# Optimization experiments

Measured on AMD Instinct MI355X. Metric: run time of the kernel, lower is better.

The kernel has to match this reference:

```python
import jax, jax.numpy as jnp
import numpy as np

SCALE = 0.08838834764831845  # 1/sqrt(128)


def setup_inputs() -> dict:
    key = jax.random.key(0)
    k1, k2, k3, k4 = jax.random.split(key, 4)
    B, Sq, H, D = 1, 2048, 32, 128
    Skv, K = 4096, 256
    return {
        "q": jax.random.normal(k1, (B, Sq, H, D), jnp.float32),
        "kv": jax.random.normal(k2, (B, Skv, 2, D), jnp.float32),  # stacked K,V (MQA)
        "attn_sink": jax.random.normal(k3, (H,), jnp.float32),
        "topk_idxs": jax.random.randint(k4, (B, Sq, K), 0, Skv),
    }


def reference(q, kv, attn_sink, topk_idxs):
    # q:        [B, Sq, H, D]
    # kv:       [B, Skv, 2, D]  (index 0 = keys, 1 = values; shared across heads)
    # topk_idxs:[B, Sq, K]      per-query selected KV positions
    # attn_sink:[H]             per-head sink logit added to the softmax denominator
    B = q.shape[0]
    # Gather selected KV per query: [B, Sq, K, 2, D]
    gathered = kv[jnp.arange(B)[:, None, None], topk_idxs]
    k = gathered[..., 0, :]  # [B, Sq, K, D]
    v = gathered[..., 1, :]  # [B, Sq, K, D]

    scores = jnp.einsum("bqhd,bqkd->bqhk", q, k) * SCALE  # [B, Sq, H, K]
    sink = attn_sink[None, None, :, None]                  # [1, 1, H, 1]

    # Numerically stable softmax over K selected tokens + sink logit.
    m = jnp.maximum(jnp.max(scores, axis=-1, keepdims=True), sink)
    e = jnp.exp(scores - m)
    denom = jnp.sum(e, axis=-1, keepdims=True) + jnp.exp(sink - m)
    probs = e / denom                                      # sink absorbs leftover mass

    out = jnp.einsum("bqhk,bqkd->bqhd", probs, v)          # [B, Sq, H, D]
    return out
```

## Files before the change

### kernel.cpp

```cpp
#include <hip/hip_runtime.h>
#include <hip/hip_bf16.h>

#define SQ 2048
#define NH 32
#define DH 128
#define NK 256
#define SCALE 0.08838834764831845f
#define LOG2E 1.4426950408889634f

typedef __attribute__((ext_vector_type(8))) __bf16 bf16x8;
typedef __attribute__((ext_vector_type(4))) float floatx4;

#define QS_STRIDE 136
#define KS_STRIDE 136
#define VB_STRIDE 72
#define PB_STRIDE 264

#define OFF_DB0  16896
#define DBSZ     18432
#define OFF_DB1  (OFF_DB0 + DBSZ)
#define OFF_RED  (OFF_DB1 + 17408)
#define OFF_RED2 (OFF_RED + 512)
#define SMEM_SZ  53760

#define SCHED_PIN() __builtin_amdgcn_sched_barrier(0)

__device__ __forceinline__ unsigned pk_bf16(float a, float b) {
  union { __hip_bfloat162 h2; unsigned u; } c;
  c.h2 = __float22bfloat162_rn(make_float2(a, b));
  return c.u;
}

__device__ __forceinline__ float fast_exp2(float x) {
#if __has_builtin(__builtin_amdgcn_exp2f)
  return __builtin_amdgcn_exp2f(x);
#else
  return exp2f(x);
#endif
}

template <int CTRL>
__device__ __forceinline__ float dpp_rot(float x) {
  int i = __builtin_bit_cast(int, x);
  i = __builtin_amdgcn_mov_dpp(i, CTRL, 0xF, 0xF, true);
  return __builtin_bit_cast(float, i);
}
#define RED16_MAX(v) { v = fmaxf(v, dpp_rot<0x121>(v)); v = fmaxf(v, dpp_rot<0x122>(v)); \
                       v = fmaxf(v, dpp_rot<0x124>(v)); v = fmaxf(v, dpp_rot<0x128>(v)); }
#define RED16_SUM(v) { v += dpp_rot<0x121>(v); v += dpp_rot<0x122>(v); \
                       v += dpp_rot<0x124>(v); v += dpp_rot<0x128>(v); }

__global__ __launch_bounds__(256) void kv_to_bf16(const float* __restrict__ kv,
                                                  unsigned short* __restrict__ kvb) {
  int i = blockIdx.x * 256 + threadIdx.x;
  float4 f = ((const float4*)kv)[i];
  uint2 o = { pk_bf16(f.x, f.y), pk_bf16(f.z, f.w) };
  ((uint2*)kvb)[i] = o;
}

struct KR { uint4 v[4]; };
struct VR { uint4 a, b, c, d; };

__device__ __forceinline__ KR k_load(const unsigned short* __restrict__ kvb,
                                     const int* __restrict__ tkg, int c, int tid) {
  int r = tid >> 2, seg = tid & 3;
  int idx = tkg[c * 64 + r];
  const uint4* p = (const uint4*)(kvb + (size_t)idx * 256 + seg * 32);
  KR k;
#pragma unroll
  for (int i = 0; i < 4; i++) k.v[i] = p[i];
  return k;
}

__device__ __forceinline__ void k_write(unsigned short* kbuf, const KR& k, int tid) {
  int r = tid >> 2, seg = tid & 3;
  uint4* d = (uint4*)&kbuf[r * KS_STRIDE + seg * 32];
#pragma unroll
  for (int i = 0; i < 4; i++) d[i] = k.v[i];
}

__device__ __forceinline__ VR v_load(const unsigned short* __restrict__ kvb,
                                     const int* __restrict__ tkg, int c, int tid) {
  int rg = tid & 15, dg = tid >> 4;
  int r0 = rg * 4, d0 = dg * 8;
  int4 i4 = *(const int4*)&tkg[c * 64 + r0];
  VR v;
  v.a = *(const uint4*)(kvb + (size_t)i4.x * 256 + 128 + d0);
  v.b = *(const uint4*)(kvb + (size_t)i4.y * 256 + 128 + d0);
  v.c = *(const uint4*)(kvb + (size_t)i4.z * 256 + 128 + d0);
  v.d = *(const uint4*)(kvb + (size_t)i4.w * 256 + 128 + d0);
  return v;
}

__device__ __forceinline__ void v_write(unsigned short* vbuf, const VR& v, int tid) {
  int rg = tid & 15, dg = tid >> 4;
  int r0 = rg * 4, d0 = dg * 8;
  const unsigned* pa = (const unsigned*)&v.a;
  const unsigned* pb = (const unsigned*)&v.b;
  const unsigned* pc = (const unsigned*)&v.c;
  const unsigned* pd = (const unsigned*)&v.d;
#pragma unroll
  for (int w = 0; w < 4; w++) {
    unsigned lo01 = __builtin_amdgcn_perm(pb[w], pa[w], 0x05040100u);
    unsigned lo23 = __builtin_amdgcn_perm(pd[w], pc[w], 0x05040100u);
    unsigned hi01 = __builtin_amdgcn_perm(pb[w], pa[w], 0x07060302u);
    unsigned hi23 = __builtin_amdgcn_perm(pd[w], pc[w], 0x07060302u);
    uint2 lo = { lo01, lo23 }, hi = { hi01, hi23 };
    *(uint2*)&vbuf[(d0 + 2 * w) * VB_STRIDE + r0] = lo;
    *(uint2*)&vbuf[(d0 + 2 * w + 1) * VB_STRIDE + r0] = hi;
  }
}

__device__ __forceinline__ void gemm1(const unsigned short* kbuf,
                                      const bf16x8 af[2][4], int nrow, int quad,
                                      floatx4& a0, floatx4& a1) {
  a0 = (floatx4){0.f, 0.f, 0.f, 0.f};
  a1 = (floatx4){0.f, 0.f, 0.f, 0.f};
  __builtin_amdgcn_s_setprio(1);
#pragma unroll
  for (int ks = 0; ks < 4; ks++) {
    bf16x8 b = *(const bf16x8*)&kbuf[nrow * KS_STRIDE + ks * 32 + quad * 8];
    a0 = __builtin_amdgcn_mfma_f32_16x16x32_bf16(af[0][ks], b, a0, 0, 0, 0);
    a1 = __builtin_amdgcn_mfma_f32_16x16x32_bf16(af[1][ks], b, a1, 0, 0, 0);
  }
  __builtin_amdgcn_s_setprio(0);
}

__device__ __forceinline__ void pv_chunk(const unsigned short* pbuf,
                                         const unsigned short* vbuf, int c,
                                         int wave, int quad, int l16,
                                         floatx4 oacc[2][2]) {
  __builtin_amdgcn_s_setprio(1);
#pragma unroll
  for (int ks = 0; ks < 2; ks++) {
    int kof = c * 64 + ks * 32 + quad * 8;
    bf16x8 a0 = *(const bf16x8*)&pbuf[l16 * PB_STRIDE + kof];
    bf16x8 a1 = *(const bf16x8*)&pbuf[(16 + l16) * PB_STRIDE + kof];
    int kl = ks * 32 + quad * 8;
    bf16x8 b0 = *(const bf16x8*)&vbuf[(wave * 32 + l16) * VB_STRIDE + kl];
    bf16x8 b1 = *(const bf16x8*)&vbuf[(wave * 32 + 16 + l16) * VB_STRIDE + kl];
    oacc[0][0] = __builtin_amdgcn_mfma_f32_16x16x32_bf16(a0, b0, oacc[0][0], 0, 0, 0);
    oacc[0][1] = __builtin_amdgcn_mfma_f32_16x16x32_bf16(a0, b1, oacc[0][1], 0, 0, 0);
    oacc[1][0] = __builtin_amdgcn_mfma_f32_16x16x32_bf16(a1, b0, oacc[1][0], 0, 0, 0);
    oacc[1][1] = __builtin_amdgcn_mfma_f32_16x16x32_bf16(a1, b1, oacc[1][1], 0, 0, 0);
  }
  __builtin_amdgcn_s_setprio(0);
}

__global__ __launch_bounds__(256, 3) void sparse_attn_kernel(
    const float* __restrict__ q, const unsigned short* __restrict__ kvb,
    const float* __restrict__ sink, const int* __restrict__ topk,
    float* __restrict__ out) {
  __shared__ __align__(16) char smem[SMEM_SZ];
  unsigned short* pbuf = (unsigned short*)smem;
  unsigned short* qs   = (unsigned short*)smem;
  unsigned short* db0  = (unsigned short*)(smem + OFF_DB0);
  unsigned short* db1  = (unsigned short*)(smem + OFF_DB1);
  float* red  = (float*)(smem + OFF_RED);
  float* red2 = (float*)(smem + OFF_RED2);

  const int tid = threadIdx.x;
  const int s = blockIdx.x;
  const int wave = tid >> 6;
  const int lane = tid & 63;
  const int quad = lane >> 4;
  const int l16 = lane & 15;
  const int* tkg = topk + (size_t)s * NK;
  unsigned short* dbuf[2] = { db0, db1 };

  {
    int r = tid >> 2, seg = tid & 3;
    int idx = tkg[r];
    const uint4* p = (const uint4*)(kvb + (size_t)idx * 256 + seg * 32);
    uint4* d = (uint4*)&db0[r * KS_STRIDE + seg * 32];
#pragma unroll
    for (int i = 0; i < 4; i++) d[i] = p[i];
  }
  KR k1 = k_load(kvb, tkg, 1, tid);
  SCHED_PIN();

  float snk[2][4];
#pragma unroll
  for (int mt = 0; mt < 2; mt++)
#pragma unroll
    for (int r = 0; r < 4; r++)
      snk[mt][r] = sink[mt * 16 + quad * 4 + r] * LOG2E;

  {
    const float QSC = SCALE * LOG2E;
    const float* qp = q + (size_t)s * (NH * DH);
    int h = tid >> 3, d0 = (tid & 7) * 16;
    const float4* src = (const float4*)(qp + h * DH + d0);
    float4 f0 = src[0], f1 = src[1], f2 = src[2], f3 = src[3];
    uint4 o0 = { pk_bf16(f0.x * QSC, f0.y * QSC), pk_bf16(f0.z * QSC, f0.w * QSC),
                 pk_bf16(f1.x * QSC, f1.y * QSC), pk_bf16(f1.z * QSC, f1.w * QSC) };
    uint4 o1 = { pk_bf16(f2.x * QSC, f2.y * QSC), pk_bf16(f2.z * QSC, f2.w * QSC),
                 pk_bf16(f3.x * QSC, f3.y * QSC), pk_bf16(f3.z * QSC, f3.w * QSC) };
    *(uint4*)&qs[h * QS_STRIDE + d0] = o0;
    *(uint4*)&qs[h * QS_STRIDE + d0 + 8] = o1;
  }
  __syncthreads();

  bf16x8 afrag[2][4];
#pragma unroll
  for (int mt = 0; mt < 2; mt++)
#pragma unroll
    for (int ks = 0; ks < 4; ks++)
      afrag[mt][ks] =
          *(const bf16x8*)&qs[(mt * 16 + l16) * QS_STRIDE + ks * 32 + quad * 8];

  const int nrow = wave * 16 + l16;

  floatx4 sc[4][2];
  KR k2 = k_load(kvb, tkg, 2, tid);
  SCHED_PIN();
  gemm1(dbuf[0], afrag, nrow, quad, sc[0][0], sc[0][1]);
  k_write(dbuf[1], k1, tid);
  __syncthreads();

  KR k3 = k_load(kvb, tkg, 3, tid);
  SCHED_PIN();
  gemm1(dbuf[1], afrag, nrow, quad, sc[1][0], sc[1][1]);
  k_write(dbuf[0], k2, tid);
  __syncthreads();

  VR v0 = v_load(kvb, tkg, 0, tid);
  SCHED_PIN();
  gemm1(dbuf[0], afrag, nrow, quad, sc[2][0], sc[2][1]);
  k_write(dbuf[1], k3, tid);
  __syncthreads();

  VR v1 = v_load(kvb, tkg, 1, tid);
  SCHED_PIN();
  gemm1(dbuf[1], afrag, nrow, quad, sc[3][0], sc[3][1]);
  v_write(dbuf[0], v0, tid);

  float mh[2][4];
#pragma unroll
  for (int mt = 0; mt < 2; mt++)
#pragma unroll
    for (int r = 0; r < 4; r++) {
      float v = fmaxf(fmaxf(sc[0][mt][r], sc[1][mt][r]),
                      fmaxf(sc[2][mt][r], sc[3][mt][r]));
      RED16_MAX(v);
      mh[mt][r] = v;
    }
  float ps[2][4];
#pragma unroll
  for (int mt = 0; mt < 2; mt++)
#pragma unroll
    for (int r = 0; r < 4; r++) {
      float acc = 0.f;
#pragma unroll
      for (int c = 0; c < 4; c++) {
        float e = fast_exp2(sc[c][mt][r] - mh[mt][r]);
        sc[c][mt][r] = e;
        acc += e;
      }
      RED16_SUM(acc);
      ps[mt][r] = acc;
    }
  if (l16 == 0) {
#pragma unroll
    for (int mt = 0; mt < 2; mt++)
#pragma unroll
      for (int r = 0; r < 4; r++) {
        red[wave * 32 + mt * 16 + quad * 4 + r]  = mh[mt][r];
        red2[wave * 32 + mt * 16 + quad * 4 + r] = ps[mt][r];
      }
  }
  __syncthreads();
  VR v2 = v_load(kvb, tkg, 2, tid);
  SCHED_PIN();
  float inv[2][4], sf[2][4];
#pragma unroll
  for (int mt = 0; mt < 2; mt++)
#pragma unroll
    for (int r = 0; r < 4; r++) {
      int h = mt * 16 + quad * 4 + r;
      float M = snk[mt][r];
#pragma unroll
      for (int w = 0; w < 4; w++) M = fmaxf(M, red[w * 32 + h]);
      float dd = fast_exp2(snk[mt][r] - M);
#pragma unroll
      for (int w = 0; w < 4; w++)
        dd += red2[w * 32 + h] * fast_exp2(red[w * 32 + h] - M);
      inv[mt][r] = 1.0f / dd;
      sf[mt][r] = fast_exp2(mh[mt][r] - M);
    }
#pragma unroll
  for (int c = 0; c < 4; c++)
#pragma unroll
    for (int mt = 0; mt < 2; mt++) {
      int col = c * 64 + wave * 16 + l16;
      unsigned short* pb = &pbuf[(mt * 16 + quad * 4) * PB_STRIDE + col];
      unsigned p01 = pk_bf16(sc[c][mt][0] * sf[mt][0], sc[c][mt][1] * sf[mt][1]);
      unsigned p23 = pk_bf16(sc[c][mt][2] * sf[mt][2], sc[c][mt][3] * sf[mt][3]);
      pb[0] = (unsigned short)p01;
      pb[PB_STRIDE] = (unsigned short)(p01 >> 16);
      pb[2 * PB_STRIDE] = (unsigned short)p23;
      pb[3 * PB_STRIDE] = (unsigned short)(p23 >> 16);
    }
  __syncthreads();

  floatx4 oacc[2][2];
#pragma unroll
  for (int mt = 0; mt < 2; mt++)
#pragma unroll
    for (int nt = 0; nt < 2; nt++)
      oacc[mt][nt] = (floatx4){0.f, 0.f, 0.f, 0.f};

  VR v3 = v_load(kvb, tkg, 3, tid);
  SCHED_PIN();
  pv_chunk(pbuf, dbuf[0], 0, wave, quad, l16, oacc);
  v_write(dbuf[1], v1, tid);
  __syncthreads();

  pv_chunk(pbuf, dbuf[1], 1, wave, quad, l16, oacc);
  v_write(dbuf[0], v2, tid);
  __syncthreads();

  pv_chunk(pbuf, dbuf[0], 2, wave, quad, l16, oacc);
  v_write(dbuf[1], v3, tid);
  __syncthreads();

  pv_chunk(pbuf, dbuf[1], 3, wave, quad, l16, oacc);

  {
    float* op = out + (size_t)s * (NH * DH);
#pragma unroll
    for (int mt = 0; mt < 2; mt++)
#pragma unroll
      for (int nt = 0; nt < 2; nt++)
#pragma unroll
        for (int r4 = 0; r4 < 4; r4++) {
          int h = mt * 16 + quad * 4 + r4;
          int d = wave * 32 + nt * 16 + l16;
          op[h * DH + d] = oacc[mt][nt][r4] * inv[mt][r4];
        }
  }
}

extern "C" void kernel_launch(void* const* d_in, const int* in_sizes, int n_in,
                              void* d_out, int out_size, void* d_ws, size_t ws_size,
                              hipStream_t stream) {
  (void)in_sizes; (void)n_in; (void)out_size; (void)ws_size;
  const float* q    = (const float*)d_in[0];
  const float* kv   = (const float*)d_in[1];
  const float* sink = (const float*)d_in[2];
  const int*   topk = (const int*)d_in[3];
  float* out = (float*)d_out;
  unsigned short* kvb = (unsigned short*)d_ws;

  kv_to_bf16<<<dim3(1024), dim3(256), 0, stream>>>(kv, kvb);
  sparse_attn_kernel<<<dim3(SQ), dim3(256), 0, stream>>>(q, kvb, sink, topk, out);
}
```

Baseline: 117.6 us.

## Load K fragments directly into registers and swizzle the probability buffer

K rows are now loaded straight from global memory into MFMA B-operand registers, with each lane fetching its own row, instead of being staged through double-buffered LDS. This removes the K LDS writes and reads plus three block barriers in the QK phase. The P buffer moves from a padded stride to an XOR-swizzled 512-byte row layout to avoid LDS bank conflicts. In exchange, register pressure rises because four K fragment sets are held at once, and the global loads are less coalesced since each lane reads 16B pieces of a gathered row.

```diff
diff --git a/kernel.cpp b/kernel.cpp
--- a/kernel.cpp
+++ b/kernel.cpp
@@ -12,18 +12,17 @@
 typedef __attribute__((ext_vector_type(4))) float floatx4;
 
 #define QS_STRIDE 136
-#define KS_STRIDE 136
 #define VB_STRIDE 72
-#define PB_STRIDE 264
-
-#define OFF_DB0  16896
-#define DBSZ     18432
-#define OFF_DB1  (OFF_DB0 + DBSZ)
-#define OFF_RED  (OFF_DB1 + 17408)
+
+#define OFF_DB0  16384
+#define OFF_DB1  (OFF_DB0 + 18432)
+#define OFF_RED  (OFF_DB1 + 18432)
 #define OFF_RED2 (OFF_RED + 512)
-#define SMEM_SZ  53760
+#define SMEM_SZ  54272
 
 #define SCHED_PIN() __builtin_amdgcn_sched_barrier(0)
+
+__device__ __forceinline__ int swz(int row) { return ((row ^ (row >> 3)) & 7) << 4; }
 
 __device__ __forceinline__ unsigned pk_bf16(float a, float b) {
   union { __hip_bfloat162 h2; unsigned u; } c;
@@ -58,26 +57,31 @@
   ((uint2*)kvb)[i] = o;
 }
 
-struct KR { uint4 v[4]; };
+struct KB { bf16x8 b[4]; };
+
+__device__ __forceinline__ KB kb_load(const unsigned short* __restrict__ kvb,
+                                      int idx, int quad) {
+  const unsigned short* kp = kvb + (size_t)idx * 256 + quad * 8;
+  KB k;
+#pragma unroll
+  for (int ks = 0; ks < 4; ks++) k.b[ks] = *(const bf16x8*)(kp + ks * 32);
+  return k;
+}
+
+__device__ __forceinline__ void gemm_reg(const KB& kb, const bf16x8 af[2][4],
+                                         floatx4& a0, floatx4& a1) {
+  a0 = (floatx4){0.f, 0.f, 0.f, 0.f};
+  a1 = (floatx4){0.f, 0.f, 0.f, 0.f};
+  __builtin_amdgcn_s_setprio(1);
+#pragma unroll
+  for (int ks = 0; ks < 4; ks++) {
+    a0 = __builtin_amdgcn_mfma_f32_16x16x32_bf16(af[0][ks], kb.b[ks], a0, 0, 0, 0);
+    a1 = __builtin_amdgcn_mfma_f32_16x16x32_bf16(af[1][ks], kb.b[ks], a1, 0, 0, 0);
+  }
+  __builtin_amdgcn_s_setprio(0);
+}
+
 struct VR { uint4 a, b, c, d; };
-
-__device__ __forceinline__ KR k_load(const unsigned short* __restrict__ kvb,
-                                     const int* __restrict__ tkg, int c, int tid) {
-  int r = tid >> 2, seg = tid & 3;
-  int idx = tkg[c * 64 + r];
-  const uint4* p = (const uint4*)(kvb + (size_t)idx * 256 + seg * 32);
-  KR k;
-#pragma unroll
-  for (int i = 0; i < 4; i++) k.v[i] = p[i];
-  return k;
-}
-
-__device__ __forceinline__ void k_write(unsigned short* kbuf, const KR& k, int tid) {
-  int r = tid >> 2, seg = tid & 3;
-  uint4* d = (uint4*)&kbuf[r * KS_STRIDE + seg * 32];
-#pragma unroll
-  for (int i = 0; i < 4; i++) d[i] = k.v[i];
-}
 
 __device__ __forceinline__ VR v_load(const unsigned short* __restrict__ kvb,
                                      const int* __restrict__ tkg, int c, int tid) {
@@ -111,31 +115,16 @@
   }
 }
 
-__device__ __forceinline__ void gemm1(const unsigned short* kbuf,
-                                      const bf16x8 af[2][4], int nrow, int quad,
-                                      floatx4& a0, floatx4& a1) {
-  a0 = (floatx4){0.f, 0.f, 0.f, 0.f};
-  a1 = (floatx4){0.f, 0.f, 0.f, 0.f};
-  __builtin_amdgcn_s_setprio(1);
-#pragma unroll
-  for (int ks = 0; ks < 4; ks++) {
-    bf16x8 b = *(const bf16x8*)&kbuf[nrow * KS_STRIDE + ks * 32 + quad * 8];
-    a0 = __builtin_amdgcn_mfma_f32_16x16x32_bf16(af[0][ks], b, a0, 0, 0, 0);
-    a1 = __builtin_amdgcn_mfma_f32_16x16x32_bf16(af[1][ks], b, a1, 0, 0, 0);
-  }
-  __builtin_amdgcn_s_setprio(0);
-}
-
-__device__ __forceinline__ void pv_chunk(const unsigned short* pbuf,
+__device__ __forceinline__ void pv_chunk(const char* pbuf,
                                          const unsigned short* vbuf, int c,
                                          int wave, int quad, int l16,
                                          floatx4 oacc[2][2]) {
   __builtin_amdgcn_s_setprio(1);
 #pragma unroll
   for (int ks = 0; ks < 2; ks++) {
-    int kof = c * 64 + ks * 32 + quad * 8;
-    bf16x8 a0 = *(const bf16x8*)&pbuf[l16 * PB_STRIDE + kof];
-    bf16x8 a1 = *(const bf16x8*)&pbuf[(16 + l16) * PB_STRIDE + kof];
+    int kof = (c * 64 + ks * 32 + quad * 8) * 2;
+    bf16x8 a0 = *(const bf16x8*)(pbuf + ((l16 * 512 + kof) ^ swz(l16)));
+    bf16x8 a1 = *(const bf16x8*)(pbuf + (((16 + l16) * 512 + kof) ^ swz(16 + l16)));
     int kl = ks * 32 + quad * 8;
     bf16x8 b0 = *(const bf16x8*)&vbuf[(wave * 32 + l16) * VB_STRIDE + kl];
     bf16x8 b1 = *(const bf16x8*)&vbuf[(wave * 32 + 16 + l16) * VB_STRIDE + kl];
@@ -152,10 +141,10 @@
     const float* __restrict__ sink, const int* __restrict__ topk,
     float* __restrict__ out) {
   __shared__ __align__(16) char smem[SMEM_SZ];
-  unsigned short* pbuf = (unsigned short*)smem;
-  unsigned short* qs   = (unsigned short*)smem;
-  unsigned short* db0  = (unsigned short*)(smem + OFF_DB0);
-  unsigned short* db1  = (unsigned short*)(smem + OFF_DB1);
+  char* pbuf = smem;
+  unsigned short* qs  = (unsigned short*)smem;
+  unsigned short* db0 = (unsigned short*)(smem + OFF_DB0);
+  unsigned short* db1 = (unsigned short*)(smem + OFF_DB1);
   float* red  = (float*)(smem + OFF_RED);
   float* red2 = (float*)(smem + OFF_RED2);
 
@@ -166,17 +155,13 @@
   const int quad = lane >> 4;
   const int l16 = lane & 15;
   const int* tkg = topk + (size_t)s * NK;
-  unsigned short* dbuf[2] = { db0, db1 };
-
-  {
-    int r = tid >> 2, seg = tid & 3;
-    int idx = tkg[r];
-    const uint4* p = (const uint4*)(kvb + (size_t)idx * 256 + seg * 32);
-    uint4* d = (uint4*)&db0[r * KS_STRIDE + seg * 32];
-#pragma unroll
-    for (int i = 0; i < 4; i++) d[i] = p[i];
-  }
-  KR k1 = k_load(kvb, tkg, 1, tid);
+  const int nrow = wave * 16 + l16;
+
+  int kidx[4];
+#pragma unroll
+  for (int c = 0; c < 4; c++) kidx[c] = tkg[c * 64 + nrow];
+  KB b0 = kb_load(kvb, kidx[0], quad);
+  KB b1 = kb_load(kvb, kidx[1], quad);
   SCHED_PIN();
 
   float snk[2][4];
@@ -209,31 +194,20 @@
       afrag[mt][ks] =
           *(const bf16x8*)&qs[(mt * 16 + l16) * QS_STRIDE + ks * 32 + quad * 8];
 
-  const int nrow = wave * 16 + l16;
-
   floatx4 sc[4][2];
-  KR k2 = k_load(kvb, tkg, 2, tid);
-  SCHED_PIN();
-  gemm1(dbuf[0], afrag, nrow, quad, sc[0][0], sc[0][1]);
-  k_write(dbuf[1], k1, tid);
-  __syncthreads();
-
-  KR k3 = k_load(kvb, tkg, 3, tid);
-  SCHED_PIN();
-  gemm1(dbuf[1], afrag, nrow, quad, sc[1][0], sc[1][1]);
-  k_write(dbuf[0], k2, tid);
-  __syncthreads();
-
+  KB b2 = kb_load(kvb, kidx[2], quad);
+  SCHED_PIN();
+  gemm_reg(b0, afrag, sc[0][0], sc[0][1]);
+  KB b3 = kb_load(kvb, kidx[3], quad);
+  SCHED_PIN();
+  gemm_reg(b1, afrag, sc[1][0], sc[1][1]);
   VR v0 = v_load(kvb, tkg, 0, tid);
   SCHED_PIN();
-  gemm1(dbuf[0], afrag, nrow, quad, sc[2][0], sc[2][1]);
-  k_write(dbuf[1], k3, tid);
-  __syncthreads();
-
+  gemm_reg(b2, afrag, sc[2][0], sc[2][1]);
   VR v1 = v_load(kvb, tkg, 1, tid);
   SCHED_PIN();
-  gemm1(dbuf[1], afrag, nrow, quad, sc[3][0], sc[3][1]);
-  v_write(dbuf[0], v0, tid);
+  gemm_reg(b3, afrag, sc[3][0], sc[3][1]);
+  v_write(db0, v0, tid);
 
   float mh[2][4];
 #pragma unroll
@@ -293,13 +267,15 @@
 #pragma unroll
     for (int mt = 0; mt < 2; mt++) {
       int col = c * 64 + wave * 16 + l16;
-      unsigned short* pb = &pbuf[(mt * 16 + quad * 4) * PB_STRIDE + col];
       unsigned p01 = pk_bf16(sc[c][mt][0] * sf[mt][0], sc[c][mt][1] * sf[mt][1]);
       unsigned p23 = pk_bf16(sc[c][mt][2] * sf[mt][2], sc[c][mt][3] * sf[mt][3]);
-      pb[0] = (unsigned short)p01;
-      pb[PB_STRIDE] = (unsigned short)(p01 >> 16);
-      pb[2 * PB_STRIDE] = (unsigned short)p23;
-      pb[3 * PB_STRIDE] = (unsigned short)(p23 >> 16);
+      unsigned short vals[4] = { (unsigned short)p01, (unsigned short)(p01 >> 16),
+                                 (unsigned short)p23, (unsigned short)(p23 >> 16) };
+#pragma unroll
+      for (int j = 0; j < 4; j++) {
+        int h = mt * 16 + quad * 4 + j;
+        *(unsigned short*)(pbuf + ((h * 512 + col * 2) ^ swz(h))) = vals[j];
+      }
     }
   __syncthreads();
 
@@ -312,19 +288,19 @@
 
   VR v3 = v_load(kvb, tkg, 3, tid);
   SCHED_PIN();
-  pv_chunk(pbuf, dbuf[0], 0, wave, quad, l16, oacc);
-  v_write(dbuf[1], v1, tid);
-  __syncthreads();
-
-  pv_chunk(pbuf, dbuf[1], 1, wave, quad, l16, oacc);
-  v_write(dbuf[0], v2, tid);
-  __syncthreads();
-
-  pv_chunk(pbuf, dbuf[0], 2, wave, quad, l16, oacc);
-  v_write(dbuf[1], v3, tid);
-  __syncthreads();
-
-  pv_chunk(pbuf, dbuf[1], 3, wave, quad, l16, oacc);
+  pv_chunk(pbuf, db0, 0, wave, quad, l16, oacc);
+  v_write(db1, v1, tid);
+  __syncthreads();
+
+  pv_chunk(pbuf, db1, 1, wave, quad, l16, oacc);
+  v_write(db0, v2, tid);
+  __syncthreads();
+
+  pv_chunk(pbuf, db0, 2, wave, quad, l16, oacc);
+  v_write(db1, v3, tid);
+  __syncthreads();
+
+  pv_chunk(pbuf, db1, 3, wave, quad, l16, oacc);
 
   {
     float* op = out + (size_t)s * (NH * DH);
```

Result: slower. 125.2 us (+6.5%).
